# Optimization experiments

Hardware: AMD Instinct MI355X
Metric: run time of the kernel (lower is better)

## Reference

```python
import jax, jax.numpy as jnp
import numpy as np


def gcn_conv(x, W, b, src, dst):
    """PyG-style GCNConv: add self-loops, symmetric normalization, then scatter-add."""
    n = x.shape[0]
    loop = jnp.arange(n, dtype=src.dtype)
    s = jnp.concatenate([src, loop])  # [E+N]
    d = jnp.concatenate([dst, loop])
    deg = jax.ops.segment_sum(jnp.ones(s.shape[0], dtype=x.dtype), d, num_segments=n)
    dinv = jax.lax.rsqrt(jnp.maximum(deg, 1.0))  # deg >= 1 due to self-loops
    norm = dinv[s] * dinv[d]                     # [E+N]
    h = x @ W                                    # [N, out]
    msg = h[s] * norm[:, None]                   # gather + scale
    return jax.ops.segment_sum(msg, d, num_segments=n) + b


def setup_inputs() -> dict:
    key = jax.random.key(0)
    ks = jax.random.split(key, 8)
    N, E, IN, H, C = 50000, 800000, 128, 64, 16
    x = jax.random.normal(ks[0], (N, IN), dtype=jnp.float32)
    edge_index = jax.random.randint(ks[1], (2, E), 0, N, dtype=jnp.int32)
    def glorot(k, shp):
        fan_in, fan_out = shp
        lim = (6.0 / (fan_in + fan_out)) ** 0.5
        return jax.random.uniform(k, shp, jnp.float32, -lim, lim)
    return {
        "x": x,
        "edge_index": edge_index,
        "W1": glorot(ks[2], (IN, H)), "b1": jnp.zeros((H,), jnp.float32),
        "W2": glorot(ks[3], (H, H)),  "b2": jnp.zeros((H,), jnp.float32),
        "Wm1": glorot(ks[4], (2 * H, H)), "bm1": jnp.zeros((H,), jnp.float32),
        "Wm2": glorot(ks[5], (H, C)),     "bm2": jnp.zeros((C,), jnp.float32),
    }


def reference(x, edge_index, W1, b1, W2, b2, Wm1, bm1, Wm2, bm2):
    src, dst = edge_index[0], edge_index[1]
    h = jax.nn.relu(gcn_conv(x, W1, b1, src, dst))
    # dropout is identity in eval mode
    h = jax.nn.relu(gcn_conv(h, W2, b2, src, dst))
    ef = jnp.concatenate([h[src], h[dst]], axis=1)  # [E, 2H]
    z = jax.nn.relu(ef @ Wm1 + bm1)
    return z @ Wm2 + bm2  # [E, numClasses]
```

## Files before the change

kernel.cpp:

```cpp
#include <hip/hip_runtime.h>
#include <hip/hip_bf16.h>

__global__ __launch_bounds__(256) void k_deg(const int* __restrict__ dst, int* __restrict__ deg, int E) {
    int e = blockIdx.x * 256 + threadIdx.x;
    if (e < E) atomicAdd(&deg[dst[e]], 1);
}

__global__ __launch_bounds__(256) void k_dinv(const int* __restrict__ deg, float* __restrict__ dinv, int N) {
    int n = blockIdx.x * 256 + threadIdx.x;
    if (n < N) dinv[n] = rsqrtf((float)(deg[n] + 1));
}

__global__ __launch_bounds__(256) void k_scan_sum(const int* __restrict__ deg, int* __restrict__ bsum, int N) {
    int n = blockIdx.x * 256 + threadIdx.x;
    int v = (n < N) ? deg[n] : 0;
#pragma unroll
    for (int o = 32; o > 0; o >>= 1) v += __shfl_down(v, o, 64);
    __shared__ int sh[4];
    if ((threadIdx.x & 63) == 0) sh[threadIdx.x >> 6] = v;
    __syncthreads();
    if (threadIdx.x == 0) bsum[blockIdx.x] = sh[0] + sh[1] + sh[2] + sh[3];
}

__global__ __launch_bounds__(256) void k_scan_off(int* __restrict__ bsum, int nb) {
    __shared__ int sh[256];
    int t = threadIdx.x;
    sh[t] = (t < nb) ? bsum[t] : 0;
    __syncthreads();
    for (int o = 1; o < 256; o <<= 1) {
        int y = (t >= o) ? sh[t - o] : 0;
        __syncthreads();
        sh[t] += y;
        __syncthreads();
    }
    if (t < nb) bsum[t] = (t == 0) ? 0 : sh[t - 1];
}

__global__ __launch_bounds__(256) void k_scan_write(const int* __restrict__ deg, const int* __restrict__ boff,
                                                    int* __restrict__ row_start, int* __restrict__ cursor, int N) {
    int n = blockIdx.x * 256 + threadIdx.x;
    int t = threadIdx.x, lane = t & 63, w = t >> 6;
    int v = (n < N) ? deg[n] : 0;
    int x = v;
#pragma unroll
    for (int o = 1; o < 64; o <<= 1) {
        int y = __shfl_up(x, o, 64);
        if (lane >= o) x += y;
    }
    __shared__ int wsum[4];
    if (lane == 63) wsum[w] = x;
    __syncthreads();
    int wo = 0;
#pragma unroll
    for (int i = 0; i < 4; ++i) wo += (i < w) ? wsum[i] : 0;
    int excl = boff[blockIdx.x] + wo + x - v;
    if (n < N) { row_start[n] = excl; cursor[n] = excl; }
    if (n == N - 1) row_start[N] = excl + v;
}

__global__ __launch_bounds__(256) void k_fill(const int* __restrict__ src, const int* __restrict__ dst,
                                              int* __restrict__ cursor, int* __restrict__ col, int E) {
    int e = blockIdx.x * 256 + threadIdx.x;
    if (e < E) {
        int d = dst[e];
        int pos = atomicAdd(&cursor[d], 1);
        col[pos] = src[e];
    }
}

__global__ __launch_bounds__(256) void k_tr(const float* __restrict__ in, float* __restrict__ outp, int R, int C) {
    int i = blockIdx.x * 256 + threadIdx.x;
    if (i < R * C) {
        int r = i / C, c = i % C;
        outp[(size_t)c * R + r] = in[(size_t)r * C + c];
    }
}

__global__ __launch_bounds__(256) void k_wpq(const float* __restrict__ Wm1, float* __restrict__ WPQ) {
    int i = blockIdx.x * 256 + threadIdx.x;
    if (i < 128 * 64) {
        int j = i >> 6, k = i & 63;
        WPQ[i] = (j < 64) ? Wm1[k * 64 + j] : Wm1[(64 + k) * 64 + (j - 64)];
    }
}

template <int K, bool RELU, bool BIAS>
__global__ __launch_bounds__(256) void k_mm_slice(const float* __restrict__ X,
                                                  const float* __restrict__ WT,
                                                  const float* __restrict__ bias,
                                                  float* __restrict__ Y, int N) {
    int n = blockIdx.x * 256 + threadIdx.x;
    int j0 = blockIdx.y * 16;
    int nc = n < N ? n : N - 1;
    const float* xr = X + (size_t)nc * K;
    const float* wr = WT + (size_t)j0 * K;
    float acc[16];
#pragma unroll
    for (int j = 0; j < 16; ++j) acc[j] = BIAS ? bias[j0 + j] : 0.f;
#pragma unroll 1
    for (int k0 = 0; k0 < K; k0 += 8) {
        float ef[8];
        *(float4*)(ef)     = *(const float4*)(xr + k0);
        *(float4*)(ef + 4) = *(const float4*)(xr + k0 + 4);
        if (RELU) {
#pragma unroll
            for (int kk = 0; kk < 8; ++kk) ef[kk] = fmaxf(ef[kk], 0.f);
        }
#pragma unroll
        for (int j = 0; j < 16; ++j) {
#pragma unroll
            for (int kk = 0; kk < 8; ++kk)
                acc[j] = fmaf(ef[kk], wr[j * K + k0 + kk], acc[j]);
        }
    }
    if (n < N) {
        float4* yp = (float4*)(Y + (size_t)n * 64 + j0);
#pragma unroll
        for (int q = 0; q < 4; ++q) yp[q] = *(float4*)(acc + q * 4);
    }
}

__global__ __launch_bounds__(256) void k_gather(const float* __restrict__ h, const float* __restrict__ dinv,
                                                const int* __restrict__ row_start, const int* __restrict__ col,
                                                const float* __restrict__ bias,
                                                float* __restrict__ a, int N) {
    int w = threadIdx.x >> 6, lane = threadIdx.x & 63;
    int d = blockIdx.x * 4 + w;
    if (d >= N) return;
    int beg = row_start[d], end = row_start[d + 1];
    float dd = dinv[d];
    float acc = fmaf(h[(size_t)d * 64 + lane], dd * dd, bias[lane]);
    int k = beg;
    for (; k + 4 <= end; k += 4) {
        int s0 = col[k], s1 = col[k + 1], s2 = col[k + 2], s3 = col[k + 3];
        float n0 = dinv[s0] * dd, n1 = dinv[s1] * dd;
        float n2 = dinv[s2] * dd, n3 = dinv[s3] * dd;
        float v0 = h[(size_t)s0 * 64 + lane], v1 = h[(size_t)s1 * 64 + lane];
        float v2 = h[(size_t)s2 * 64 + lane], v3 = h[(size_t)s3 * 64 + lane];
        acc = fmaf(v0, n0, acc);
        acc = fmaf(v1, n1, acc);
        acc = fmaf(v2, n2, acc);
        acc = fmaf(v3, n3, acc);
    }
    for (; k < end; ++k) {
        int s = col[k];
        acc = fmaf(h[(size_t)s * 64 + lane], dinv[s] * dd, acc);
    }
    a[(size_t)d * 64 + lane] = acc;
}

__global__ __launch_bounds__(256) void k_p_inplace(float* __restrict__ A2P,
                                                   const float* __restrict__ WPQ,
                                                   const float* __restrict__ bm1, int N) {
    int n = blockIdx.x * 256 + threadIdx.x;
    int nc = n < N ? n : N - 1;
    const float* xr = A2P + (size_t)nc * 64;
    float acc[64];
#pragma unroll
    for (int j = 0; j < 64; ++j) acc[j] = bm1[j];
#pragma unroll 1
    for (int k0 = 0; k0 < 64; k0 += 8) {
        float ef[8];
        *(float4*)(ef)     = *(const float4*)(xr + k0);
        *(float4*)(ef + 4) = *(const float4*)(xr + k0 + 4);
#pragma unroll
        for (int kk = 0; kk < 8; ++kk) ef[kk] = fmaxf(ef[kk], 0.f);
#pragma unroll
        for (int j = 0; j < 64; ++j)
#pragma unroll
            for (int kk = 0; kk < 8; ++kk)
                acc[j] = fmaf(ef[kk], WPQ[j * 64 + k0 + kk], acc[j]);
    }
    if (n < N) {
#pragma unroll
        for (int q = 0; q < 16; ++q)
            *(float4*)(A2P + (size_t)n * 64 + q * 4) = *(float4*)(acc + q * 4);
    }
}

__global__ __launch_bounds__(256) void k_edge_pq(const float* __restrict__ P,
                                                 const float* __restrict__ Q,
                                                 const int* __restrict__ src,
                                                 const int* __restrict__ dst,
                                                 const float* __restrict__ W2T,
                                                 const float* __restrict__ bm2,
                                                 float* __restrict__ out, int E) {
    int e = blockIdx.x * 256 + threadIdx.x;
    int ec = e < E ? e : E - 1;
    int s = src[ec], d = dst[ec];
    const float4* p4 = (const float4*)(P + (size_t)s * 64);
    const float4* q4 = (const float4*)(Q + (size_t)d * 64);
    float z[64];
#pragma unroll
    for (int c = 0; c < 16; ++c) {
        float4 a = p4[c], b = q4[c];
        z[c * 4 + 0] = fmaxf(a.x + b.x, 0.f);
        z[c * 4 + 1] = fmaxf(a.y + b.y, 0.f);
        z[c * 4 + 2] = fmaxf(a.z + b.z, 0.f);
        z[c * 4 + 3] = fmaxf(a.w + b.w, 0.f);
    }
    float o[16];
#pragma unroll
    for (int c = 0; c < 16; ++c) {
        float a = bm2[c];
#pragma unroll
        for (int j = 0; j < 64; ++j) a = fmaf(z[j], W2T[c * 64 + j], a);
        o[c] = a;
    }
    if (e < E) {
        float4* op = (float4*)(out + (size_t)e * 16);
#pragma unroll
        for (int q = 0; q < 4; ++q) op[q] = *(float4*)(o + q * 4);
    }
}

extern "C" void kernel_launch(void* const* d_in, const int* in_sizes, int n_in,
                              void* d_out, int out_size, void* d_ws, size_t ws_size,
                              hipStream_t stream) {
    const float* x   = (const float*)d_in[0];
    const int* ei    = (const int*)d_in[1];
    const float* W1  = (const float*)d_in[2];
    const float* b1  = (const float*)d_in[3];
    const float* W2  = (const float*)d_in[4];
    const float* b2  = (const float*)d_in[5];
    const float* Wm1 = (const float*)d_in[6];
    const float* bm1 = (const float*)d_in[7];
    const float* Wm2 = (const float*)d_in[8];
    const float* bm2 = (const float*)d_in[9];
    float* out = (float*)d_out;

    const int H  = in_sizes[3];
    const int IN = in_sizes[2] / H;
    const int N  = in_sizes[0] / IN;
    const int E  = in_sizes[1] / 2;
    const int* src = ei;
    const int* dst = ei + E;

    char* ws = (char*)d_ws;
    size_t off = 0;
    auto alloc = [&](size_t bytes) { void* p = ws + off; off += (bytes + 255) & ~(size_t)255; return p; };
    float* dinv = (float*)alloc((size_t)N * 4);
    float* W1T  = (float*)alloc((size_t)IN * H * 4);
    float* W2T  = (float*)alloc((size_t)H * H * 4);
    float* WPQ  = (float*)alloc((size_t)2 * H * H * 4);
    float* Wm2T = (float*)alloc((size_t)H * 16 * 4);
    float* bufB = (float*)alloc((size_t)N * 64 * 4);
    float* Qbuf = (float*)alloc((size_t)N * 64 * 4);
    float* PbufSep = (float*)alloc((size_t)N * 64 * 4);
    const bool fastP = (off <= ws_size);
    float* bufA = (float*)d_out;
    float* Pbuf = fastP ? PbufSep : bufB;

    const int Npad = (N + 255) & ~255;
    int* degtmp = (int*)Qbuf;
    int* rowst  = degtmp + Npad;
    int* cursor = rowst + Npad;
    int* bsum   = cursor + Npad;
    int* col    = bsum + 256;

    const int NBn = (N + 255) / 256;
    const int NBe = (E + 255) / 256;
    const int NG  = (N + 3) / 4;

    hipMemsetAsync(degtmp, 0, (size_t)N * sizeof(int), stream);
    k_deg<<<NBe, 256, 0, stream>>>(dst, degtmp, E);
    k_dinv<<<NBn, 256, 0, stream>>>(degtmp, dinv, N);
    k_scan_sum<<<NBn, 256, 0, stream>>>(degtmp, bsum, N);
    k_scan_off<<<1, 256, 0, stream>>>(bsum, NBn);
    k_scan_write<<<NBn, 256, 0, stream>>>(degtmp, bsum, rowst, cursor, N);
    k_fill<<<NBe, 256, 0, stream>>>(src, dst, cursor, col, E);

    k_tr<<<(IN * H + 255) / 256, 256, 0, stream>>>(W1, W1T, IN, H);
    k_tr<<<(H * H + 255) / 256, 256, 0, stream>>>(W2, W2T, H, H);
    k_tr<<<(H * 16 + 255) / 256, 256, 0, stream>>>(Wm2, Wm2T, H, 16);
    k_wpq<<<(2 * H * H + 255) / 256, 256, 0, stream>>>(Wm1, WPQ);

    const dim3 G4(NBn, 4);

    k_mm_slice<128, false, false><<<G4, 256, 0, stream>>>(x, W1T, nullptr, bufA, N);
    k_gather<<<NG, 256, 0, stream>>>(bufA, dinv, rowst, col, b1, bufB, N);

    k_mm_slice<64, true, false><<<G4, 256, 0, stream>>>(bufB, W2T, nullptr, bufA, N);
    k_gather<<<NG, 256, 0, stream>>>(bufA, dinv, rowst, col, b2, bufB, N);

    k_mm_slice<64, true, false><<<G4, 256, 0, stream>>>(bufB, WPQ + 64 * 64, nullptr, Qbuf, N);
    if (fastP) {
        k_mm_slice<64, true, true><<<G4, 256, 0, stream>>>(bufB, WPQ, bm1, PbufSep, N);
    } else {
        k_p_inplace<<<NBn, 256, 0, stream>>>(bufB, WPQ, bm1, N);
    }

    k_edge_pq<<<NBe, 256, 0, stream>>>(Pbuf, Qbuf, src, dst, Wm2T, bm2, out, E);
}
```

Baseline: 451.1 us.

## Process edge MLP in dst-sorted CSR order with (src, eid) pairs

The CSR fill now stores (src, edge id) pairs, or edge ids only when workspace is tight, instead of bare source indices. The final edge MLP kernel walks edges in destination-sorted CSR order, so consecutive threads share the same Q row, and finds each destination by binary search over row_start. Results are scattered back to the original edge positions. The aim is better cache locality for Q reads, paid for with a binary search per edge, scattered output writes, and larger item loads in the gather kernels.

```diff
diff --git a/kernel.cpp b/kernel.cpp
--- a/kernel.cpp
+++ b/kernel.cpp
@@ -58,13 +58,15 @@
     if (n == N - 1) row_start[N] = excl + v;
 }
 
+template <bool PAIR>
 __global__ __launch_bounds__(256) void k_fill(const int* __restrict__ src, const int* __restrict__ dst,
-                                              int* __restrict__ cursor, int* __restrict__ col, int E) {
+                                              int* __restrict__ cursor, void* __restrict__ item, int E) {
     int e = blockIdx.x * 256 + threadIdx.x;
     if (e < E) {
         int d = dst[e];
         int pos = atomicAdd(&cursor[d], 1);
-        col[pos] = src[e];
+        if (PAIR) ((int2*)item)[pos] = make_int2(src[e], e);
+        else      ((int*)item)[pos] = e;
     }
 }
 
@@ -120,8 +122,10 @@
     }
 }
 
+template <bool PAIR>
 __global__ __launch_bounds__(256) void k_gather(const float* __restrict__ h, const float* __restrict__ dinv,
-                                                const int* __restrict__ row_start, const int* __restrict__ col,
+                                                const int* __restrict__ row_start, const void* __restrict__ item,
+                                                const int* __restrict__ srcArr,
                                                 const float* __restrict__ bias,
                                                 float* __restrict__ a, int N) {
     int w = threadIdx.x >> 6, lane = threadIdx.x & 63;
@@ -132,7 +136,16 @@
     float acc = fmaf(h[(size_t)d * 64 + lane], dd * dd, bias[lane]);
     int k = beg;
     for (; k + 4 <= end; k += 4) {
-        int s0 = col[k], s1 = col[k + 1], s2 = col[k + 2], s3 = col[k + 3];
+        int s0, s1, s2, s3;
+        if (PAIR) {
+            const int2* it = (const int2*)item;
+            int2 p0 = it[k], p1 = it[k + 1], p2 = it[k + 2], p3 = it[k + 3];
+            s0 = p0.x; s1 = p1.x; s2 = p2.x; s3 = p3.x;
+        } else {
+            const int* eid = (const int*)item;
+            int e0 = eid[k], e1 = eid[k + 1], e2 = eid[k + 2], e3 = eid[k + 3];
+            s0 = srcArr[e0]; s1 = srcArr[e1]; s2 = srcArr[e2]; s3 = srcArr[e3];
+        }
         float n0 = dinv[s0] * dd, n1 = dinv[s1] * dd;
         float n2 = dinv[s2] * dd, n3 = dinv[s3] * dd;
         float v0 = h[(size_t)s0 * 64 + lane], v1 = h[(size_t)s1 * 64 + lane];
@@ -143,7 +156,9 @@
         acc = fmaf(v3, n3, acc);
     }
     for (; k < end; ++k) {
-        int s = col[k];
+        int s;
+        if (PAIR) s = ((const int2*)item)[k].x;
+        else      s = srcArr[((const int*)item)[k]];
         acc = fmaf(h[(size_t)s * 64 + lane], dinv[s] * dd, acc);
     }
     a[(size_t)d * 64 + lane] = acc;
@@ -208,6 +223,56 @@
         o[c] = a;
     }
     if (e < E) {
+        float4* op = (float4*)(out + (size_t)e * 16);
+#pragma unroll
+        for (int q = 0; q < 4; ++q) op[q] = *(float4*)(o + q * 4);
+    }
+}
+
+template <bool PAIR>
+__global__ __launch_bounds__(256) void k_edge_csr(const float* __restrict__ P,
+                                                  const float* __restrict__ Q,
+                                                  const int* __restrict__ rowst,
+                                                  const void* __restrict__ item,
+                                                  const int* __restrict__ srcArr,
+                                                  const float* __restrict__ W2T,
+                                                  const float* __restrict__ bm2,
+                                                  float* __restrict__ out, int E, int N) {
+    int i = blockIdx.x * 256 + threadIdx.x;
+    int ic = i < E ? i : E - 1;
+    int s, e;
+    if (PAIR) {
+        int2 pe = ((const int2*)item)[ic];
+        s = pe.x; e = pe.y;
+    } else {
+        e = ((const int*)item)[ic];
+        s = srcArr[e];
+    }
+    int lo = 0, hi = N - 1;
+    while (lo < hi) {
+        int mid = (lo + hi + 1) >> 1;
+        if (rowst[mid] <= ic) lo = mid; else hi = mid - 1;
+    }
+    const float4* p4 = (const float4*)(P + (size_t)s * 64);
+    const float4* q4 = (const float4*)(Q + (size_t)lo * 64);
+    float z[64];
+#pragma unroll
+    for (int c = 0; c < 16; ++c) {
+        float4 a = p4[c], b = q4[c];
+        z[c * 4 + 0] = fmaxf(a.x + b.x, 0.f);
+        z[c * 4 + 1] = fmaxf(a.y + b.y, 0.f);
+        z[c * 4 + 2] = fmaxf(a.z + b.z, 0.f);
+        z[c * 4 + 3] = fmaxf(a.w + b.w, 0.f);
+    }
+    float o[16];
+#pragma unroll
+    for (int c = 0; c < 16; ++c) {
+        float a = bm2[c];
+#pragma unroll
+        for (int j = 0; j < 64; ++j) a = fmaf(z[j], W2T[c * 64 + j], a);
+        o[c] = a;
+    }
+    if (i < E) {
         float4* op = (float4*)(out + (size_t)e * 16);
 #pragma unroll
         for (int q = 0; q < 4; ++q) op[q] = *(float4*)(o + q * 4);
@@ -236,39 +301,75 @@
     const int* src = ei;
     const int* dst = ei + E;
 
+    auto al = [](size_t b) { return (b + 255) & ~(size_t)255; };
     char* ws = (char*)d_ws;
+
+    const size_t wb     = al((size_t)IN * H * 4) + al((size_t)H * H * 4) + al((size_t)2 * H * H * 4) + al((size_t)H * 16 * 4);
+    const size_t rowstB = al(((size_t)N + 1) * 4);
+    const size_t nodeB  = al((size_t)N * 64 * 4);
+    const size_t pairB  = al((size_t)E * 8);
+    const size_t eidB   = al((size_t)E * 4);
+    const size_t needA  = wb + rowstB + pairB + 3 * nodeB;
+    const size_t needB  = wb + rowstB + eidB  + 3 * nodeB;
+
+    const int tier = (needA <= ws_size) ? 0 : (needB <= ws_size) ? 1 : 2;
+
+    float *W1T, *W2T, *WPQ, *Wm2T, *bufB, *Qbuf, *Pbuf, *dinv;
+    int *deg, *rowst, *cursor, *bsum;
+    void* item;
+    float* bufA = (float*)d_out;
+    bool slicedP = true;
+
     size_t off = 0;
-    auto alloc = [&](size_t bytes) { void* p = ws + off; off += (bytes + 255) & ~(size_t)255; return p; };
-    float* dinv = (float*)alloc((size_t)N * 4);
-    float* W1T  = (float*)alloc((size_t)IN * H * 4);
-    float* W2T  = (float*)alloc((size_t)H * H * 4);
-    float* WPQ  = (float*)alloc((size_t)2 * H * H * 4);
-    float* Wm2T = (float*)alloc((size_t)H * 16 * 4);
-    float* bufB = (float*)alloc((size_t)N * 64 * 4);
-    float* Qbuf = (float*)alloc((size_t)N * 64 * 4);
-    float* PbufSep = (float*)alloc((size_t)N * 64 * 4);
-    const bool fastP = (off <= ws_size);
-    float* bufA = (float*)d_out;
-    float* Pbuf = fastP ? PbufSep : bufB;
-
-    const int Npad = (N + 255) & ~255;
-    int* degtmp = (int*)Qbuf;
-    int* rowst  = degtmp + Npad;
-    int* cursor = rowst + Npad;
-    int* bsum   = cursor + Npad;
-    int* col    = bsum + 256;
+    auto alc = [&](size_t b) { void* p = ws + off; off += al(b); return p; };
+
+    if (tier <= 1) {
+        W1T  = (float*)alc((size_t)IN * H * 4);
+        W2T  = (float*)alc((size_t)H * H * 4);
+        WPQ  = (float*)alc((size_t)2 * H * H * 4);
+        Wm2T = (float*)alc((size_t)H * 16 * 4);
+        rowst = (int*)alc(((size_t)N + 1) * 4);
+        item  = alc(tier == 0 ? (size_t)E * 8 : (size_t)E * 4);
+        bufB = (float*)alc((size_t)N * 64 * 4);
+        Qbuf = (float*)alc((size_t)N * 64 * 4);
+        Pbuf = (float*)alc((size_t)N * 64 * 4);
+        char* pz = (char*)Pbuf;
+        dinv   = (float*)pz;
+        deg    = (int*)(pz + al((size_t)N * 4));
+        cursor = (int*)(pz + 2 * al((size_t)N * 4));
+        bsum   = (int*)(pz + 3 * al((size_t)N * 4));
+    } else {
+        dinv = (float*)alc((size_t)N * 4);
+        W1T  = (float*)alc((size_t)IN * H * 4);
+        W2T  = (float*)alc((size_t)H * H * 4);
+        WPQ  = (float*)alc((size_t)2 * H * H * 4);
+        Wm2T = (float*)alc((size_t)H * 16 * 4);
+        bufB = (float*)alc((size_t)N * 64 * 4);
+        Qbuf = (float*)alc((size_t)N * 64 * 4);
+        float* PbufSep = (float*)alc((size_t)N * 64 * 4);
+        slicedP = (off <= ws_size);
+        Pbuf = slicedP ? PbufSep : bufB;
+        char* qz = (char*)Qbuf;
+        size_t qo = 0;
+        deg    = (int*)(qz + qo); qo += al((size_t)N * 4);
+        rowst  = (int*)(qz + qo); qo += al(((size_t)N + 1) * 4);
+        cursor = (int*)(qz + qo); qo += al((size_t)N * 4);
+        bsum   = (int*)(qz + qo); qo += al(1024);
+        item   = (void*)(qz + qo);
+    }
 
     const int NBn = (N + 255) / 256;
     const int NBe = (E + 255) / 256;
     const int NG  = (N + 3) / 4;
 
-    hipMemsetAsync(degtmp, 0, (size_t)N * sizeof(int), stream);
-    k_deg<<<NBe, 256, 0, stream>>>(dst, degtmp, E);
-    k_dinv<<<NBn, 256, 0, stream>>>(degtmp, dinv, N);
-    k_scan_sum<<<NBn, 256, 0, stream>>>(degtmp, bsum, N);
+    hipMemsetAsync(deg, 0, (size_t)N * sizeof(int), stream);
+    k_deg<<<NBe, 256, 0, stream>>>(dst, deg, E);
+    k_dinv<<<NBn, 256, 0, stream>>>(deg, dinv, N);
+    k_scan_sum<<<NBn, 256, 0, stream>>>(deg, bsum, N);
     k_scan_off<<<1, 256, 0, stream>>>(bsum, NBn);
-    k_scan_write<<<NBn, 256, 0, stream>>>(degtmp, bsum, rowst, cursor, N);
-    k_fill<<<NBe, 256, 0, stream>>>(src, dst, cursor, col, E);
+    k_scan_write<<<NBn, 256, 0, stream>>>(deg, bsum, rowst, cursor, N);
+    if (tier == 1) k_fill<false><<<NBe, 256, 0, stream>>>(src, dst, cursor, item, E);
+    else           k_fill<true ><<<NBe, 256, 0, stream>>>(src, dst, cursor, item, E);
 
     k_tr<<<(IN * H + 255) / 256, 256, 0, stream>>>(W1, W1T, IN, H);
     k_tr<<<(H * H + 255) / 256, 256, 0, stream>>>(W2, W2T, H, H);
@@ -278,17 +379,18 @@
     const dim3 G4(NBn, 4);
 
     k_mm_slice<128, false, false><<<G4, 256, 0, stream>>>(x, W1T, nullptr, bufA, N);
-    k_gather<<<NG, 256, 0, stream>>>(bufA, dinv, rowst, col, b1, bufB, N);
+    if (tier == 1) k_gather<false><<<NG, 256, 0, stream>>>(bufA, dinv, rowst, item, src, b1, bufB, N);
+    else           k_gather<true ><<<NG, 256, 0, stream>>>(bufA, dinv, rowst, item, src, b1, bufB, N);
 
     k_mm_slice<64, true, false><<<G4, 256, 0, stream>>>(bufB, W2T, nullptr, bufA, N);
-    k_gather<<<NG, 256, 0, stream>>>(bufA, dinv, rowst, col, b2, bufB, N);
+    if (tier == 1) k_gather<false><<<NG, 256, 0, stream>>>(bufA, dinv, rowst, item, src, b2, bufB, N);
+    else           k_gather<true ><<<NG, 256, 0, stream>>>(bufA, dinv, rowst, item, src, b2, bufB, N);
 
     k_mm_slice<64, true, false><<<G4, 256, 0, stream>>>(bufB, WPQ + 64 * 64, nullptr, Qbuf, N);
-    if (fastP) {
-        k_mm_slice<64, true, true><<<G4, 256, 0, stream>>>(bufB, WPQ, bm1, PbufSep, N);
-    } else {
-        k_p_inplace<<<NBn, 256, 0, stream>>>(bufB, WPQ, bm1, N);
-    }
-
-    k_edge_pq<<<NBe, 256, 0, stream>>>(Pbuf, Qbuf, src, dst, Wm2T, bm2, out, E);
-}
+    if (slicedP) k_mm_slice<64, true, true><<<G4, 256, 0, stream>>>(bufB, WPQ, bm1, Pbuf, N);
+    else         k_p_inplace<<<NBn, 256, 0, stream>>>(bufB, WPQ, bm1, N);
+
+    if (tier == 0)      k_edge_csr<true ><<<NBe, 256, 0, stream>>>(Pbuf, Qbuf, rowst, item, src, Wm2T, bm2, out, E, N);
+    else if (tier == 1) k_edge_csr<false><<<NBe, 256, 0, stream>>>(Pbuf, Qbuf, rowst, item, src, Wm2T, bm2, out, E, N);
+    else                k_edge_pq<<<NBe, 256, 0, stream>>>(Pbuf, Qbuf, src, dst, Wm2T, bm2, out, E);
+}
```

After: 431.6 us. 4.3% less time.
